# Kernel tuning notes

Measured on AMD Instinct MI355X. Metric: run time of the kernel, lower is better.

The kernel has to match this reference:

```python
import jax, jax.numpy as jnp
import numpy as np

B, T, FDIM, H = 8, 2048, 512, 8
DK = FDIM // H
INF_VAL = 10000.0


def setup_inputs() -> dict:
    key = jax.random.key(0)
    ks = jax.random.split(key, 12)
    s = 1.0 / np.sqrt(FDIM)
    return {
        "query": jax.random.normal(ks[0], (B, T, FDIM), jnp.float32),
        "key": jax.random.normal(ks[1], (B, T, FDIM), jnp.float32),
        "value": jax.random.normal(ks[2], (B, T, FDIM), jnp.float32),
        "mask": jax.random.bernoulli(ks[3], 0.1, (B, T, T)),
        "Wq": jax.random.normal(ks[4], (FDIM, FDIM), jnp.float32) * s,
        "bq": jnp.zeros((FDIM,), jnp.float32),
        "Wk": jax.random.normal(ks[5], (FDIM, FDIM), jnp.float32) * s,
        "bk": jnp.zeros((FDIM,), jnp.float32),
        "Wv": jax.random.normal(ks[6], (FDIM, FDIM), jnp.float32) * s,
        "bv": jnp.zeros((FDIM,), jnp.float32),
        "Wo": jax.random.normal(ks[7], (FDIM, FDIM), jnp.float32) * s,
        "bo": jnp.zeros((FDIM,), jnp.float32),
    }


def reference(query, key, value, mask, Wq, bq, Wk, bk, Wv, bv, Wo, bo):
    # Linear projections (torch Linear: y = x W^T + b) then split heads.
    q = (query @ Wq.T + bq).reshape(B, T, H, DK).transpose(0, 2, 1, 3)  # (B,H,T1,DK)
    k = (key @ Wk.T + bk).reshape(B, T, H, DK).transpose(0, 2, 1, 3)    # (B,H,T2,DK)
    v = (value @ Wv.T + bv).reshape(B, T, H, DK).transpose(0, 2, 1, 3)  # (B,H,T2,DK)
    scores = jnp.einsum("bhqd,bhkd->bhqk", q, k) / jnp.sqrt(jnp.float32(DK))
    m = mask[:, None, :, :]  # (B,1,T1,T2)
    scores = jnp.where(m, -INF_VAL, scores)
    attn = jax.nn.softmax(scores, axis=-1)
    attn = jnp.where(m, 0.0, attn)
    # dropout_rate = 0.0 -> identity
    x = jnp.einsum("bhqk,bhkd->bhqd", attn, v)  # (B,H,T1,DK)
    x = x.transpose(0, 2, 1, 3).reshape(B, T, H * DK)
    return x @ Wo.T + bo
```

## Files before the change

### kernel.cpp

```cpp
#include <hip/hip_runtime.h>
#include <hip/hip_bf16.h>
#include <stdint.h>

#define B_N 8
#define T_N 2048
#define FDIM_N 512
#define H_N 8
#define DK_N 64

typedef float f32x4 __attribute__((ext_vector_type(4)));
typedef float float4v __attribute__((ext_vector_type(4)));
typedef __bf16 bf16x8 __attribute__((ext_vector_type(8)));
typedef unsigned short ushort8v __attribute__((ext_vector_type(8)));
typedef unsigned int uint2v __attribute__((ext_vector_type(2)));
typedef unsigned int uint4v __attribute__((ext_vector_type(4)));

#if __has_builtin(__builtin_amdgcn_exp2f)
#define EXP2F(x) __builtin_amdgcn_exp2f(x)
#else
#define EXP2F(x) exp2f(x)
#endif

static __device__ __forceinline__ unsigned short f2bf(float f) {
  unsigned int u = __builtin_bit_cast(unsigned int, f);
  u += 0x7fffu + ((u >> 16) & 1u);
  return (unsigned short)(u >> 16);
}

static __device__ __forceinline__ unsigned cvtpk(float lo, float hi) {
  unsigned r;
  asm("v_cvt_pk_bf16_f32 %0, %1, %2" : "=v"(r) : "v"(lo), "v"(hi));
  return r;
}

static __device__ __forceinline__ void gld_lds16(const void* g, void* l) {
  __builtin_amdgcn_global_load_lds(
      (const __attribute__((address_space(1))) unsigned int*)g,
      (__attribute__((address_space(3))) unsigned int*)l, 16, 0, 0);
}

static __device__ __forceinline__ bf16x8 ld_bf8(const unsigned short* p) {
  return *reinterpret_cast<const bf16x8*>(p);
}

#define SWZ8(row, colE) ((colE) ^ (((row) & 7) << 3))

#define QSCALE 0.1803368801111244f

__global__ __launch_bounds__(256) void prep_k(
    const int* __restrict__ m, const float* __restrict__ w0, const float* __restrict__ w1,
    const float* __restrict__ w2, const float* __restrict__ w3,
    const float* __restrict__ qin, const float* __restrict__ kin, const float* __restrict__ vin,
    unsigned short* __restrict__ wb, unsigned short* __restrict__ qb,
    unsigned short* __restrict__ kb, unsigned short* __restrict__ vb,
    unsigned long long* __restrict__ mbits) {
  const int bid = blockIdx.x;
  if (bid < 2048) {
    const size_t n = (size_t)B_N * T_N * T_N;
    const size_t stride = (size_t)2048 * 256;
    for (size_t i = (size_t)bid * 256 + threadIdx.x; i < n; i += stride) {
      unsigned long long bl = __ballot(m[i] != 0);
      if ((threadIdx.x & 63) == 0) mbits[i >> 6] = bl;
    }
  } else if (bid < 2560) {
    const int i = (bid - 2048) * 256 + threadIdx.x;
    const int ws = i >> 15, o = i & 32767;
    const float* w = (ws == 0) ? w0 : (ws == 1) ? w1 : (ws == 2) ? w2 : w3;
    const float4v a = *reinterpret_cast<const float4v*>(w + (size_t)o * 8);
    const float4v b = *reinterpret_cast<const float4v*>(w + (size_t)o * 8 + 4);
    const ushort8v out = {f2bf(a.x), f2bf(a.y), f2bf(a.z), f2bf(a.w),
                          f2bf(b.x), f2bf(b.y), f2bf(b.z), f2bf(b.w)};
    *reinterpret_cast<ushort8v*>(wb + (size_t)i * 8) = out;
  } else {
    const unsigned total = 3u << 20;
    const unsigned stride = 1536u * 256u;
    for (unsigned i = (bid - 2560) * 256 + threadIdx.x; i < total; i += stride) {
      const unsigned sel = i >> 20, off = i & 0xFFFFFu;
      const float* in = (sel == 0) ? qin : (sel == 1) ? kin : vin;
      unsigned short* out = (sel == 0) ? qb : (sel == 1) ? kb : vb;
      const float4v a = *reinterpret_cast<const float4v*>(in + (size_t)off * 8);
      const float4v b = *reinterpret_cast<const float4v*>(in + (size_t)off * 8 + 4);
      const ushort8v o = {f2bf(a.x), f2bf(a.y), f2bf(a.z), f2bf(a.w),
                          f2bf(b.x), f2bf(b.y), f2bf(b.z), f2bf(b.w)};
      *reinterpret_cast<ushort8v*>(out + (size_t)off * 8) = o;
    }
  }
}

template <int MODE>
__global__ __launch_bounds__(256, 3) void gemm_bt_k(const unsigned short* __restrict__ Ap,
                                                    const unsigned short* __restrict__ Wp,
                                                    const float* __restrict__ biasp,
                                                    void* __restrict__ Cp) {
  __shared__ unsigned short As[128 * 64];
  __shared__ unsigned short Bs[128 * 64];
  const int tid = threadIdx.x;
  const int lane = tid & 63, w = tid >> 6;
  const int lr = lane & 15, lg = lane >> 4;
  const int id = blockIdx.x;
  const int work = (id & 7) * 64 + (id >> 3);
  const int m0 = (work >> 2) * 128, n0 = (work & 3) * 128;
  const int wm = (w & 1) * 64, wn = (w >> 1) * 64;
  const int swz_rd = (lr & 7) << 3;

  f32x4 acc[4][4];
  const f32x4 z4 = {0.f, 0.f, 0.f, 0.f};
#pragma unroll
  for (int i = 0; i < 4; ++i)
#pragma unroll
    for (int j = 0; j < 4; ++j) acc[i][j] = z4;

  for (int k0 = 0; k0 < 512; k0 += 64) {
    __syncthreads();
#pragma unroll
    for (int i = 0; i < 4; ++i) {
      const int c = i * 256 + tid;
      const int row = c >> 3, ch = c & 7;
      const int sw = SWZ8(row, ch * 8);
      gld_lds16(Ap + (size_t)(m0 + row) * 512 + k0 + sw, &As[c * 8]);
      gld_lds16(Wp + (size_t)(n0 + row) * 512 + k0 + sw, &Bs[c * 8]);
    }
    __syncthreads();
    bf16x8 af[4][2], bw[4][2];
#pragma unroll
    for (int mt = 0; mt < 4; ++mt)
#pragma unroll
      for (int kk = 0; kk < 2; ++kk)
        af[mt][kk] = ld_bf8(&As[(wm + mt * 16 + lr) * 64 + ((kk * 32 + lg * 8) ^ swz_rd)]);
#pragma unroll
    for (int nt = 0; nt < 4; ++nt)
#pragma unroll
      for (int kk = 0; kk < 2; ++kk)
        bw[nt][kk] = ld_bf8(&Bs[(wn + nt * 16 + lr) * 64 + ((kk * 32 + lg * 8) ^ swz_rd)]);
#pragma unroll
    for (int kk = 0; kk < 2; ++kk)
#pragma unroll
      for (int mt = 0; mt < 4; ++mt)
#pragma unroll
        for (int nt = 0; nt < 4; ++nt)
          acc[mt][nt] =
              __builtin_amdgcn_mfma_f32_16x16x32_bf16(af[mt][kk], bw[nt][kk], acc[mt][nt], 0, 0, 0);
  }

#pragma unroll
  for (int nt = 0; nt < 4; ++nt) {
    const int n = n0 + wn + nt * 16 + lr;
    const float bias = biasp[n];
#pragma unroll
    for (int mt = 0; mt < 4; ++mt) {
#pragma unroll
      for (int j = 0; j < 4; ++j) {
        const int m = m0 + wm + mt * 16 + lg * 4 + j;
        float v = acc[mt][nt][j] + bias;
        const int bb = m >> 11, t = m & 2047;
        const int hh = n >> 6, d = n & 63;
        if constexpr (MODE == 0) {
          v *= QSCALE;
          ((unsigned short*)Cp)[(((size_t)(bb * 8 + hh) * 2048 + t) << 6) + d] = f2bf(v);
        } else if constexpr (MODE == 1) {
          ((unsigned short*)Cp)[(((size_t)(bb * 8 + hh) * 2048 + t) << 6) + d] = f2bf(v);
        } else if constexpr (MODE == 2) {
          const int tp = (t & ~31) | (((t >> 2) & 3) << 3) | (((t >> 4) & 1) << 2) | (t & 3);
          ((unsigned short*)Cp)[(((size_t)(bb * 8 + hh) * 64 + d) << 11) + tp] = f2bf(v);
        } else {
          ((float*)Cp)[(size_t)m * 512 + n] = v;
        }
      }
    }
  }
}

__global__ __launch_bounds__(512, 4) void attn_k(
    const unsigned short* __restrict__ qg, const unsigned short* __restrict__ kg,
    const unsigned short* __restrict__ vtg, const unsigned long long* __restrict__ mb,
    unsigned short* __restrict__ xg) {
  __shared__ unsigned short Ks[2][64 * 64];
  __shared__ unsigned short Vts[2][64 * 64];

  const int tid = threadIdx.x;
  const int lane = tid & 63, w = tid >> 6;
  const int lr = lane & 15, lg = lane >> 4;
  const int swz_rd = (lr & 7) << 3;
  const int id = blockIdx.x;
  const int work = (id & 7) * 128 + (id >> 3);
  const int bh = work >> 4, qt0 = work & 15;
  const int b = bh >> 3, h = bh & 7;
  const int q0 = qt0 * 128;

  bf16x8 aq[2];
#pragma unroll
  for (int kk = 0; kk < 2; ++kk)
    aq[kk] = ld_bf8(qg + ((size_t)bh * T_N + q0 + w * 16 + lr) * DK_N + kk * 32 + lg * 8);

  const int krow = tid >> 3, kch = tid & 7;
  const unsigned short* kp =
      kg + (size_t)bh * (T_N * DK_N) + krow * 64 + SWZ8(krow, kch * 8);
  const unsigned short* vp =
      vtg + ((size_t)bh * DK_N + krow) * T_N + SWZ8(krow, kch * 8);
  const unsigned long long* mp = mb + ((size_t)b * T_N + q0 + w * 16 + lr) * (T_N / 64);

  f32x4 OT[4];
  float rsacc = 0.f;
  const f32x4 z4 = {0.f, 0.f, 0.f, 0.f};
#pragma unroll
  for (int dt = 0; dt < 4; ++dt) OT[dt] = z4;

  f32x4 ST[4];
  bf16x8 pfrag[2];
  unsigned long long mc, mn = 0;

#define STAGE(PB)                        \
  {                                      \
    gld_lds16(kp, &Ks[PB][tid * 8]);     \
    gld_lds16(vp, &Vts[PB][tid * 8]);    \
    kp += 4096; vp += 64;                \
  }

#define QKT_BLOCK(CUR)                                                                      \
  {                                                                                         \
    __builtin_amdgcn_s_setprio(1);                                                          \
    _Pragma("unroll") for (int st = 0; st < 4; ++st) {                                      \
      const bf16x8 kb0 = ld_bf8(&Ks[CUR][(st * 16 + lr) * 64 + ((lg * 8) ^ swz_rd)]);       \
      const bf16x8 kb1 = ld_bf8(&Ks[CUR][(st * 16 + lr) * 64 + ((32 + lg * 8) ^ swz_rd)]);  \
      f32x4 a_ = __builtin_amdgcn_mfma_f32_16x16x32_bf16(kb0, aq[0], z4, 0, 0, 0);          \
      ST[st] = __builtin_amdgcn_mfma_f32_16x16x32_bf16(kb1, aq[1], a_, 0, 0, 0);            \
    }                                                                                       \
    __builtin_amdgcn_s_setprio(0);                                                          \
  }

#define SOFTMAX_BLOCK()                                                                     \
  {                                                                                         \
    float sv[4][4];                                                                         \
    _Pragma("unroll") for (int st = 0; st < 4; ++st) {                                      \
      const unsigned nib = (unsigned)(mc >> (st * 16 + lg * 4)) & 0xFu;                     \
      _Pragma("unroll") for (int j = 0; j < 4; ++j) {                                       \
        float e = EXP2F(ST[st][j]);                                                         \
        e = ((nib >> j) & 1u) ? 0.f : e;                                                    \
        sv[st][j] = e;                                                                      \
      }                                                                                     \
    }                                                                                       \
    rsacc += (((sv[0][0] + sv[0][1]) + (sv[0][2] + sv[0][3])) +                             \
              ((sv[1][0] + sv[1][1]) + (sv[1][2] + sv[1][3]))) +                            \
             (((sv[2][0] + sv[2][1]) + (sv[2][2] + sv[2][3])) +                             \
              ((sv[3][0] + sv[3][1]) + (sv[3][2] + sv[3][3])));                             \
    uint4v pk0_, pk1_;                                                                      \
    pk0_.x = cvtpk(sv[0][0], sv[0][1]); pk0_.y = cvtpk(sv[0][2], sv[0][3]);                 \
    pk0_.z = cvtpk(sv[1][0], sv[1][1]); pk0_.w = cvtpk(sv[1][2], sv[1][3]);                 \
    pk1_.x = cvtpk(sv[2][0], sv[2][1]); pk1_.y = cvtpk(sv[2][2], sv[2][3]);                 \
    pk1_.z = cvtpk(sv[3][0], sv[3][1]); pk1_.w = cvtpk(sv[3][2], sv[3][3]);                 \
    pfrag[0] = __builtin_bit_cast(bf16x8, pk0_);                                            \
    pfrag[1] = __builtin_bit_cast(bf16x8, pk1_);                                            \
  }

#define PV_BLOCK(PRV)                                                                       \
  {                                                                                         \
    __builtin_amdgcn_s_setprio(1);                                                          \
    _Pragma("unroll") for (int dt = 0; dt < 4; ++dt) {                                      \
      const bf16x8 v0 = ld_bf8(&Vts[PRV][(dt * 16 + lr) * 64 + ((lg * 8) ^ swz_rd)]);       \
      const bf16x8 v1 = ld_bf8(&Vts[PRV][(dt * 16 + lr) * 64 + ((32 + lg * 8) ^ swz_rd)]);  \
      f32x4 o_ = __builtin_amdgcn_mfma_f32_16x16x32_bf16(v0, pfrag[0], OT[dt], 0, 0, 0);    \
      OT[dt] = __builtin_amdgcn_mfma_f32_16x16x32_bf16(v1, pfrag[1], o_, 0, 0, 0);          \
    }                                                                                       \
    __builtin_amdgcn_s_setprio(0);                                                          \
  }

  STAGE(0);
  mc = mp[0];
  __syncthreads();
  QKT_BLOCK(0);
  STAGE(1);
  mn = mp[1];
  SOFTMAX_BLOCK();
  mc = mn;

#define ITER(KT, CUR, LAST)            \
  {                                    \
    PV_BLOCK(CUR ^ 1);                 \
    __syncthreads();                   \
    QKT_BLOCK(CUR);                    \
    if (!(LAST)) {                     \
      STAGE(CUR ^ 1);                  \
      mn = mp[(KT) + 1];               \
    }                                  \
    SOFTMAX_BLOCK();                   \
    mc = mn;                           \
  }

  ITER(1, 1, 0)
  for (int kt0 = 2; kt0 < 30; kt0 += 2) {
    ITER(kt0, 0, 0)
    ITER(kt0 + 1, 1, 0)
  }
  ITER(30, 0, 0)
  ITER(31, 1, 1)
  PV_BLOCK(1);
#undef ITER
#undef STAGE
#undef QKT_BLOCK
#undef SOFTMAX_BLOCK
#undef PV_BLOCK

  {
    float l = rsacc;
    l += __shfl_xor(l, 16);
    l += __shfl_xor(l, 32);
    const float inv = (l > 0.f) ? 1.f / l : 0.f;
    const int q = q0 + w * 16 + lr;
#pragma unroll
    for (int dt = 0; dt < 4; ++dt) {
      uint2v o;
      o.x = cvtpk(OT[dt][0] * inv, OT[dt][1] * inv);
      o.y = cvtpk(OT[dt][2] * inv, OT[dt][3] * inv);
      *reinterpret_cast<uint2v*>(xg + ((size_t)(b * T_N + q)) * FDIM_N + h * 64 + dt * 16 +
                                 lg * 4) = o;
    }
  }
}

extern "C" void kernel_launch(void* const* d_in, const int* in_sizes, int n_in,
                              void* d_out, int out_size, void* d_ws, size_t ws_size,
                              hipStream_t stream) {
  const float* query = (const float*)d_in[0];
  const float* key = (const float*)d_in[1];
  const float* value = (const float*)d_in[2];
  const int* mask = (const int*)d_in[3];
  const float* Wq = (const float*)d_in[4];
  const float* bq = (const float*)d_in[5];
  const float* Wk = (const float*)d_in[6];
  const float* bk = (const float*)d_in[7];
  const float* Wv = (const float*)d_in[8];
  const float* bv = (const float*)d_in[9];
  const float* Wo = (const float*)d_in[10];
  const float* bo = (const float*)d_in[11];

  const size_t NE = (size_t)16384 * 512;
  const size_t WE = (size_t)512 * 512;
  unsigned short* qb_in = (unsigned short*)d_ws;
  unsigned short* kb_in = qb_in + NE;
  unsigned short* vb_in = kb_in + NE;
  unsigned short* wqb = vb_in + NE;
  unsigned short* q_scr = wqb + 4 * WE;
  unsigned short* k_scr = q_scr + NE;
  unsigned short* vT_scr = k_scr + NE;
  unsigned long long* mbits = (unsigned long long*)(vT_scr + NE);
  unsigned short* x_scr = qb_in;

  prep_k<<<4096, 256, 0, stream>>>(mask, Wq, Wk, Wv, Wo, query, key, value, wqb, qb_in, kb_in,
                                   vb_in, mbits);
  gemm_bt_k<0><<<512, 256, 0, stream>>>(qb_in, wqb + 0 * WE, bq, q_scr);
  gemm_bt_k<1><<<512, 256, 0, stream>>>(kb_in, wqb + 1 * WE, bk, k_scr);
  gemm_bt_k<2><<<512, 256, 0, stream>>>(vb_in, wqb + 2 * WE, bv, vT_scr);
  attn_k<<<1024, 512, 0, stream>>>(q_scr, k_scr, vT_scr, mbits, x_scr);
  gemm_bt_k<3><<<512, 256, 0, stream>>>(x_scr, wqb + 3 * WE, bo, (float*)d_out);
}
```

Baseline: 214.8 us.

## Deepen K/V LDS pipeline to four buffers with one barrier per two tiles

Replaces the double-buffered K and V shared-memory tiles with a four-slot ring in a single LDS array and prefetches two tiles ahead. The loop is restructured so a __syncthreads is issued every two key tiles instead of every tile. Per-lane LDS read addresses are precomputed once so each slot is reached by a constant offset. This raises LDS use to 64 KB per block, which may lower occupancy under the 4-blocks launch bound.

```diff
diff --git a/kernel.cpp b/kernel.cpp
--- a/kernel.cpp
+++ b/kernel.cpp
@@ -174,8 +174,7 @@
     const unsigned short* __restrict__ qg, const unsigned short* __restrict__ kg,
     const unsigned short* __restrict__ vtg, const unsigned long long* __restrict__ mb,
     unsigned short* __restrict__ xg) {
-  __shared__ unsigned short Ks[2][64 * 64];
-  __shared__ unsigned short Vts[2][64 * 64];
+  __shared__ unsigned short L[4 * 8192];
 
   const int tid = threadIdx.x;
   const int lane = tid & 63, w = tid >> 6;
@@ -192,6 +191,13 @@
   for (int kk = 0; kk < 2; ++kk)
     aq[kk] = ld_bf8(qg + ((size_t)bh * T_N + q0 + w * 16 + lr) * DK_N + kk * 32 + lg * 8);
 
+  const unsigned short* rp[8];
+#pragma unroll
+  for (int st = 0; st < 4; ++st) {
+    rp[2 * st + 0] = &L[(st * 16 + lr) * 64 + ((lg * 8) ^ swz_rd)];
+    rp[2 * st + 1] = &L[(st * 16 + lr) * 64 + ((32 + lg * 8) ^ swz_rd)];
+  }
+
   const int krow = tid >> 3, kch = tid & 7;
   const unsigned short* kp =
       kg + (size_t)bh * (T_N * DK_N) + krow * 64 + SWZ8(krow, kch * 8);
@@ -207,32 +213,32 @@
 
   f32x4 ST[4];
   bf16x8 pfrag[2];
-  unsigned long long mc, mn = 0;
-
-#define STAGE(PB)                        \
-  {                                      \
-    gld_lds16(kp, &Ks[PB][tid * 8]);     \
-    gld_lds16(vp, &Vts[PB][tid * 8]);    \
-    kp += 4096; vp += 64;                \
-  }
-
-#define QKT_BLOCK(CUR)                                                                      \
+  unsigned long long mA, mB;
+
+#define STG(B_)                                       \
+  {                                                   \
+    gld_lds16(kp, &L[(B_) * 8192 + tid * 8]);         \
+    gld_lds16(vp, &L[(B_) * 8192 + 4096 + tid * 8]);  \
+    kp += 4096; vp += 64;                             \
+  }
+
+#define QKT(B_)                                                                             \
   {                                                                                         \
     __builtin_amdgcn_s_setprio(1);                                                          \
     _Pragma("unroll") for (int st = 0; st < 4; ++st) {                                      \
-      const bf16x8 kb0 = ld_bf8(&Ks[CUR][(st * 16 + lr) * 64 + ((lg * 8) ^ swz_rd)]);       \
-      const bf16x8 kb1 = ld_bf8(&Ks[CUR][(st * 16 + lr) * 64 + ((32 + lg * 8) ^ swz_rd)]);  \
+      const bf16x8 kb0 = ld_bf8(rp[2 * st + 0] + (B_) * 8192);                              \
+      const bf16x8 kb1 = ld_bf8(rp[2 * st + 1] + (B_) * 8192);                              \
       f32x4 a_ = __builtin_amdgcn_mfma_f32_16x16x32_bf16(kb0, aq[0], z4, 0, 0, 0);          \
       ST[st] = __builtin_amdgcn_mfma_f32_16x16x32_bf16(kb1, aq[1], a_, 0, 0, 0);            \
     }                                                                                       \
     __builtin_amdgcn_s_setprio(0);                                                          \
   }
 
-#define SOFTMAX_BLOCK()                                                                     \
+#define SM(MREG)                                                                            \
   {                                                                                         \
     float sv[4][4];                                                                         \
     _Pragma("unroll") for (int st = 0; st < 4; ++st) {                                      \
-      const unsigned nib = (unsigned)(mc >> (st * 16 + lg * 4)) & 0xFu;                     \
+      const unsigned nib = (unsigned)((MREG) >> (st * 16 + lg * 4)) & 0xFu;                 \
       _Pragma("unroll") for (int j = 0; j < 4; ++j) {                                       \
         float e = EXP2F(ST[st][j]);                                                         \
         e = ((nib >> j) & 1u) ? 0.f : e;                                                    \
@@ -252,53 +258,59 @@
     pfrag[1] = __builtin_bit_cast(bf16x8, pk1_);                                            \
   }
 
-#define PV_BLOCK(PRV)                                                                       \
+#define PV(B_)                                                                              \
   {                                                                                         \
     __builtin_amdgcn_s_setprio(1);                                                          \
     _Pragma("unroll") for (int dt = 0; dt < 4; ++dt) {                                      \
-      const bf16x8 v0 = ld_bf8(&Vts[PRV][(dt * 16 + lr) * 64 + ((lg * 8) ^ swz_rd)]);       \
-      const bf16x8 v1 = ld_bf8(&Vts[PRV][(dt * 16 + lr) * 64 + ((32 + lg * 8) ^ swz_rd)]);  \
+      const bf16x8 v0 = ld_bf8(rp[2 * dt + 0] + (B_) * 8192 + 4096);                        \
+      const bf16x8 v1 = ld_bf8(rp[2 * dt + 1] + (B_) * 8192 + 4096);                        \
       f32x4 o_ = __builtin_amdgcn_mfma_f32_16x16x32_bf16(v0, pfrag[0], OT[dt], 0, 0, 0);    \
       OT[dt] = __builtin_amdgcn_mfma_f32_16x16x32_bf16(v1, pfrag[1], o_, 0, 0, 0);          \
     }                                                                                       \
     __builtin_amdgcn_s_setprio(0);                                                          \
   }
 
-  STAGE(0);
-  mc = mp[0];
+  STG(0); STG(1);
+  mA = mp[0]; mB = mp[1];
+  const unsigned long long* mload = mp + 3;
   __syncthreads();
-  QKT_BLOCK(0);
-  STAGE(1);
-  mn = mp[1];
-  SOFTMAX_BLOCK();
-  mc = mn;
-
-#define ITER(KT, CUR, LAST)            \
-  {                                    \
-    PV_BLOCK(CUR ^ 1);                 \
-    __syncthreads();                   \
-    QKT_BLOCK(CUR);                    \
-    if (!(LAST)) {                     \
-      STAGE(CUR ^ 1);                  \
-      mn = mp[(KT) + 1];               \
-    }                                  \
-    SOFTMAX_BLOCK();                   \
-    mc = mn;                           \
-  }
-
-  ITER(1, 1, 0)
-  for (int kt0 = 2; kt0 < 30; kt0 += 2) {
-    ITER(kt0, 0, 0)
-    ITER(kt0 + 1, 1, 0)
-  }
-  ITER(30, 0, 0)
-  ITER(31, 1, 1)
-  PV_BLOCK(1);
-#undef ITER
-#undef STAGE
-#undef QKT_BLOCK
-#undef SOFTMAX_BLOCK
-#undef PV_BLOCK
+  QKT(0); STG(2); SM(mA); mA = mp[2];
+
+#define ITER2A                                                              \
+  {                                                                                         \
+    PV(0); __syncthreads();                                                                 \
+    QKT(1); STG(3); SM(mB); mB = mload[0];                                                  \
+    PV(1);                                                                                  \
+    QKT(2); STG(0); SM(mA); mA = mload[1]; mload += 2;                                      \
+  }
+#define ITER2B                                                              \
+  {                                                                                         \
+    PV(2); __syncthreads();                                                                 \
+    QKT(3); STG(1); SM(mB); mB = mload[0];                                                  \
+    PV(3);                                                                                  \
+    QKT(0); STG(2); SM(mA); mA = mload[1]; mload += 2;                                      \
+  }
+
+  for (int i = 0; i < 7; ++i) {
+    ITER2A;
+    ITER2B;
+  }
+  {
+    PV(0); __syncthreads();
+    QKT(1); STG(3); SM(mB); mB = mload[0];
+    PV(1);
+    QKT(2); SM(mA);
+  }
+  PV(2);
+  __syncthreads();
+  QKT(3); SM(mB);
+  PV(3);
+#undef ITER2A
+#undef ITER2B
+#undef STG
+#undef QKT
+#undef SM
+#undef PV
 
   {
     float l = rsacc;
```

After: 213.7 us. Within noise of the previous version (-0.5%).
